# Performance work log

Hardware: AMD Instinct MI355X
Metric: run time of the kernel (lower is better)

Reference implementation:

```python
import jax, jax.numpy as jnp
import numpy as np

# Dimensions (TinyLlama-like)
B, T = 4, 1024
D = 2048          # hidden_size
H, DH = 32, 64    # heads, head_dim
HK = 8            # kv heads (GQA, n_rep = 4)
RQ, RKV = 32, 32  # per-head SVD ranks
RO, RF = 1024, 1024
I = 5632          # intermediate_size
THETA = 10000.0
EPS = 1e-5


def setup_inputs() -> dict:
    key = jax.random.key(0)
    ks = jax.random.split(key, 16)
    p = lambda k, s: jax.random.normal(k, s, jnp.float32) * 0.02
    return {
        "x": jax.random.normal(ks[0], (B, T, D), jnp.float32),
        "ln1_w": jnp.ones((D,), jnp.float32),
        "ln2_w": jnp.ones((D,), jnp.float32),
        "q_Us": p(ks[1], (H, DH, RQ)),  "q_V": p(ks[2], (H, RQ, D)),
        "k_Us": p(ks[3], (HK, DH, RKV)), "k_V": p(ks[4], (HK, RKV, D)),
        "v_Us": p(ks[5], (HK, DH, RKV)), "v_V": p(ks[6], (HK, RKV, D)),
        "o_Us": p(ks[7], (D, RO)),  "o_V": p(ks[8], (RO, H * DH)),
        "g_Us": p(ks[9], (I, RF)),  "g_V": p(ks[10], (RF, D)),
        "u_Us": p(ks[11], (I, RF)), "u_V": p(ks[12], (RF, D)),
        "d_Us": p(ks[13], (D, RF)), "d_V": p(ks[14], (RF, I)),
    }


def _rms(x, w):
    return x * jax.lax.rsqrt(jnp.mean(x * x, axis=-1, keepdims=True) + EPS) * w


def _rope_cos_sin(t_len, dh, dtype):
    half = dh // 2
    inv_freq = 1.0 / (THETA ** (jnp.arange(half, dtype=jnp.float32) / half))
    ang = jnp.arange(t_len, dtype=jnp.float32)[:, None] * inv_freq[None, :]  # [T, half]
    return jnp.cos(ang).astype(dtype), jnp.sin(ang).astype(dtype)


def _apply_rope(x, cos, sin):
    # x: [B,h,T,Dh], LLaMA half-split rotation
    half = x.shape[-1] // 2
    x1, x2 = x[..., :half], x[..., half:]
    c = cos[None, None]  # [1,1,T,half]
    s = sin[None, None]
    return jnp.concatenate([x1 * c - x2 * s, x2 * c + x1 * s], axis=-1)


def reference(x, ln1_w, ln2_w, q_Us, q_V, k_Us, k_V, v_Us, v_V,
              o_Us, o_V, g_Us, g_V, u_Us, u_V, d_Us, d_V):
    b, t, d = x.shape
    h1 = _rms(x, ln1_w)

    # per-head low-rank projections: y_h = x @ V_h^T @ Us_h^T
    q = jnp.einsum('bhtr,hdr->bhtd', jnp.einsum('btD,hrD->bhtr', h1, q_V), q_Us)  # [B,H,T,Dh]
    k = jnp.einsum('bhtr,hdr->bhtd', jnp.einsum('btD,hrD->bhtr', h1, k_V), k_Us)  # [B,Hk,T,Dh]
    v = jnp.einsum('bhtr,hdr->bhtd', jnp.einsum('btD,hrD->bhtr', h1, v_V), v_Us)

    cos, sin = _rope_cos_sin(t, DH, x.dtype)
    q = _apply_rope(q, cos, sin)
    k = _apply_rope(k, cos, sin)

    n_rep = H // HK
    k = jnp.repeat(k, n_rep, axis=1)  # _repeat_kv
    v = jnp.repeat(v, n_rep, axis=1)

    scale = 1.0 / np.sqrt(DH)
    scores = jnp.einsum('bhtd,bhsd->bhts', q, k) * scale
    causal = jnp.tril(jnp.ones((t, t), bool))
    scores = jnp.where(causal[None, None], scores, jnp.finfo(scores.dtype).min)
    attn = jax.nn.softmax(scores, axis=-1)
    ctx = jnp.einsum('bhts,bhsd->bhtd', attn, v)
    ctx = ctx.transpose(0, 2, 1, 3).reshape(b, t, H * DH)

    # low-rank output proj: o = ctx @ o_V^T @ o_Us^T
    attn_out = jnp.einsum('btr,Dr->btD', jnp.einsum('btk,rk->btr', ctx, o_V), o_Us)
    x = x + attn_out

    # SwiGLU MLP with low-rank factors
    h2 = _rms(x, ln2_w)
    g = jnp.einsum('btr,ir->bti', jnp.einsum('btD,rD->btr', h2, g_V), g_Us)
    u = jnp.einsum('btr,ir->bti', jnp.einsum('btD,rD->btr', h2, u_V), u_Us)
    ff = jax.nn.silu(g) * u
    down = jnp.einsum('btr,Dr->btD', jnp.einsum('bti,ri->btr', ff, d_V), d_Us)
    return x + down
```

## Files before the change

kernel.cpp:

```cpp
#include <hip/hip_runtime.h>
#include <math.h>

typedef unsigned short u16;
typedef unsigned int u32;
typedef __bf16 bf16x8 __attribute__((ext_vector_type(8)));
typedef float f32x4 __attribute__((ext_vector_type(4)));

__device__ __forceinline__ float bf2f(u16 u) {
  union { u32 i; float f; } x; x.i = ((u32)u) << 16; return x.f;
}
__device__ __forceinline__ u16 f2bf(float f) {
  union { float f; u32 i; } x; x.f = f;
  return (u16)((x.i + 0x7fffu + ((x.i >> 16) & 1u)) >> 16);
}

#define GLDS16(gp, lp)                                                        \
  __builtin_amdgcn_global_load_lds(                                           \
      (const __attribute__((address_space(1))) u32*)(gp),                     \
      (__attribute__((address_space(3))) u32*)(lp), 16, 0, 0)

__global__ void detect_k(const u16* __restrict__ w, int* __restrict__ flag) {
  if (threadIdx.x == 0 && blockIdx.x == 0)
    *flag = (w[0] == 0x0000u && w[1] == 0x3F80u) ? 1 : 0;
}

struct CvtArgs {
  const void* src[17];
  u32 dstOff[17];
  u32 blkOff[18];
};

__global__ __launch_bounds__(256) void cvt_all(CvtArgs a, u16* __restrict__ dstB,
                                               const int* __restrict__ flag) {
  int seg = 0;
  const int bx = blockIdx.x;
#pragma unroll 1
  while (bx >= (int)a.blkOff[seg + 1]) seg++;
  const long local = ((long)(bx - a.blkOff[seg]) * 256 + threadIdx.x) * 8;
  u16* dst = dstB + a.dstOff[seg] + local;
  if (*flag) {
    const float* s = (const float*)a.src[seg] + local;
    float4 va = *(const float4*)(s);
    float4 vb = *(const float4*)(s + 4);
    uint4 o; u16* op = (u16*)&o;
    op[0] = f2bf(va.x); op[1] = f2bf(va.y); op[2] = f2bf(va.z); op[3] = f2bf(va.w);
    op[4] = f2bf(vb.x); op[5] = f2bf(vb.y); op[6] = f2bf(vb.z); op[7] = f2bf(vb.w);
    *(uint4*)dst = o;
  } else {
    *(uint4*)dst = *(const uint4*)((const u16*)a.src[seg] + local);
  }
}

__global__ __launch_bounds__(256) void rms_k(const u16* __restrict__ x,
                                             const u16* __restrict__ w,
                                             u16* __restrict__ out) {
  const long row = blockIdx.x;
  const u16* xr = x + row * 2048;
  u16* orow = out + row * 2048;
  const int tid = threadIdx.x;
  const int base = tid * 8;
  uint4 u = *(const uint4*)(xr + base);
  const u16* us = (const u16*)&u;
  float v[8];
  float ss = 0.f;
#pragma unroll
  for (int i = 0; i < 8; i++) { v[i] = bf2f(us[i]); ss += v[i] * v[i]; }
#pragma unroll
  for (int off = 32; off > 0; off >>= 1) ss += __shfl_xor(ss, off);
  __shared__ float red[4];
  if ((tid & 63) == 0) red[tid >> 6] = ss;
  __syncthreads();
  float total = red[0] + red[1] + red[2] + red[3];
  float inv = rsqrtf(total * (1.0f / 2048.0f) + 1e-5f);
  uint4 wv = *(const uint4*)(w + base);
  const u16* wp = (const u16*)&wv;
  uint4 o;
  u16* op = (u16*)&o;
#pragma unroll
  for (int i = 0; i < 8; i++) op[i] = f2bf(v[i] * inv * bf2f(wp[i]));
  *(uint4*)(orow + base) = o;
}

template <int EPI>
__global__ __launch_bounds__(256, 2) void gemm_bt(const u16* __restrict__ A,
                                                  const u16* __restrict__ B,
                                                  void* Cv,
                                                  const u16* R,
                                                  const int* flagp,
                                                  int N, int Klen, int lda, int ldb) {
  __shared__ u16 As[128 * 32];
  __shared__ u16 Bs[128 * 32];
  const int m0 = blockIdx.y * 128;
  const int n0 = blockIdx.x * 128;
  const int tid = threadIdx.x;
  const int wave = tid >> 6;
  const int lane = tid & 63;
  const int wr = (wave >> 1) * 64;
  const int wc = (wave & 1) * 64;
  const int l16 = lane & 15;
  const int quad = lane >> 4;
  u16* C = (u16*)Cv;
  float* Cf = (float*)Cv;
  bool f32o = false;
  if (EPI == 3) f32o = (*flagp != 0);

  f32x4 acc[4][4];
#pragma unroll
  for (int i = 0; i < 4; i++)
#pragma unroll
    for (int j = 0; j < 4; j++) acc[i][j] = (f32x4){0.f, 0.f, 0.f, 0.f};

  const int srow = wave * 16 + (lane >> 2);
  const int scol = (lane & 3) * 8;
  const u16* Ag = A + (long)(m0 + srow) * lda + scol;
  const u16* Bg = B + (long)(n0 + srow) * ldb + scol;
  const long astep = (long)64 * lda;
  const long bstep = (long)64 * ldb;
  u16* Asw = &As[wave * 16 * 32];
  u16* Bsw = &Bs[wave * 16 * 32];

  for (int k0 = 0; k0 < Klen; k0 += 32) {
    GLDS16(Ag + k0, Asw);
    GLDS16(Ag + astep + k0, Asw + 64 * 32);
    GLDS16(Bg + k0, Bsw);
    GLDS16(Bg + bstep + k0, Bsw + 64 * 32);
    __syncthreads();
    bf16x8 af[4], bfr[4];
#pragma unroll
    for (int t = 0; t < 4; t++) {
      af[t]  = *(const bf16x8*)(&As[(wr + t * 16 + l16) * 32 + quad * 8]);
      bfr[t] = *(const bf16x8*)(&Bs[(wc + t * 16 + l16) * 32 + quad * 8]);
    }
#pragma unroll
    for (int i = 0; i < 4; i++)
#pragma unroll
      for (int j = 0; j < 4; j++)
        acc[i][j] = __builtin_amdgcn_mfma_f32_16x16x32_bf16(bfr[j], af[i], acc[i][j], 0, 0, 0);
    __syncthreads();
  }

#pragma unroll
  for (int i = 0; i < 4; i++) {
    const int m = m0 + wr + i * 16 + l16;
#pragma unroll
    for (int j = 0; j < 4; j++) {
      const int n = n0 + wc + j * 16 + quad * 4;
      const long idx = (long)m * N + n;
      float v[4];
#pragma unroll
      for (int r = 0; r < 4; r++) v[r] = acc[i][j][r];
      if (EPI == 1 || EPI == 3) {
        uint2 rr = *(const uint2*)(R + idx);
        const u16* rp = (const u16*)&rr;
#pragma unroll
        for (int r = 0; r < 4; r++) v[r] += bf2f(rp[r]);
      }
      if (EPI == 3 && f32o) {
        float4 o = {v[0], v[1], v[2], v[3]};
        *(float4*)(Cf + idx) = o;
      } else {
        uint2 o; u16* op = (u16*)&o;
#pragma unroll
        for (int r = 0; r < 4; r++) op[r] = f2bf(v[r]);
        *(uint2*)(C + idx) = o;
      }
    }
  }
}

#define STAGE_SILU(buf, k0)                                                   \
  do {                                                                        \
    GLDS16(Ag_ + (k0), &SH[buf][0][woff]);                                    \
    GLDS16(Au_ + (k0), &SH[buf][1][woff]);                                    \
    GLDS16(Bg_ + (k0), &SH[buf][2][woff]);                                    \
    GLDS16(Bu_ + (k0), &SH[buf][3][woff]);                                    \
  } while (0)

__global__ __launch_bounds__(512, 4) void gemm_silu(const u16* __restrict__ Agp,
                                                    const u16* __restrict__ Aup,
                                                    const u16* __restrict__ Bgp,
                                                    const u16* __restrict__ Bup,
                                                    u16* __restrict__ C,
                                                    int N, int Klen, int lda, int ldb) {
  __shared__ u16 SH[2][4][128 * 32];
  const int m0 = blockIdx.y * 128;
  const int n0 = blockIdx.x * 128;
  const int tid = threadIdx.x;
  const int wave = tid >> 6;
  const int lane = tid & 63;
  const int wid = wave & 3;
  const int isU = wave >> 2;
  const int wr = (wid >> 1) * 64;
  const int wc = (wid & 1) * 64;
  const int l16 = lane & 15;
  const int quad = lane >> 4;
  const int matA = isU;
  const int matB = 2 + isU;

  f32x4 acc[4][4];
#pragma unroll
  for (int i = 0; i < 4; i++)
#pragma unroll
    for (int j = 0; j < 4; j++) acc[i][j] = (f32x4){0.f, 0.f, 0.f, 0.f};

  const int srow = wave * 16 + (lane >> 2);
  const int scol = ((lane & 3) ^ ((lane >> 3) & 3)) * 8;
  const u16* Ag_ = Agp + (long)(m0 + srow) * lda + scol;
  const u16* Au_ = Aup + (long)(m0 + srow) * lda + scol;
  const u16* Bg_ = Bgp + (long)(n0 + srow) * ldb + scol;
  const u16* Bu_ = Bup + (long)(n0 + srow) * ldb + scol;
  const int woff = wave * 512;
  const int rsw = (quad ^ ((l16 >> 1) & 3)) * 8;

  const int nk = Klen >> 5;
  STAGE_SILU(0, 0);
  int cur = 0;
  for (int kt = 0; kt < nk; ++kt) {
    if (kt + 1 < nk) {
      STAGE_SILU(cur ^ 1, (kt + 1) << 5);
      asm volatile("s_waitcnt vmcnt(4)" ::: "memory");
    } else {
      asm volatile("s_waitcnt vmcnt(0)" ::: "memory");
    }
    asm volatile("s_barrier" ::: "memory");
    bf16x8 af[4], bfr[4];
#pragma unroll
    for (int t = 0; t < 4; t++) {
      af[t]  = *(const bf16x8*)(&SH[cur][matA][(wr + t * 16 + l16) * 32 + rsw]);
      bfr[t] = *(const bf16x8*)(&SH[cur][matB][(wc + t * 16 + l16) * 32 + rsw]);
    }
#pragma unroll
    for (int i = 0; i < 4; i++)
#pragma unroll
      for (int j = 0; j < 4; j++)
        acc[i][j] = __builtin_amdgcn_mfma_f32_16x16x32_bf16(bfr[j], af[i], acc[i][j], 0, 0, 0);
    asm volatile("s_barrier" ::: "memory");
    cur ^= 1;
  }

  float* xch = (float*)&SH[0][0][0];
  if (isU) {
    float* w = xch + wid * 4096 + lane * 4;
#pragma unroll
    for (int i = 0; i < 4; i++)
#pragma unroll
      for (int j = 0; j < 4; j++)
        *(f32x4*)(w + (i * 4 + j) * 256) = acc[i][j];
  }
  __syncthreads();
  if (!isU) {
    const float* w = xch + wid * 4096 + lane * 4;
#pragma unroll
    for (int i = 0; i < 4; i++) {
      const int m = m0 + wr + i * 16 + l16;
#pragma unroll
      for (int j = 0; j < 4; j++) {
        const int n = n0 + wc + j * 16 + quad * 4;
        const long idx = (long)m * N + n;
        f32x4 uv = *(const f32x4*)(w + (i * 4 + j) * 256);
        uint2 o; u16* op = (u16*)&o;
#pragma unroll
        for (int r = 0; r < 4; r++) {
          float g = acc[i][j][r];
          float v = uv[r] * g / (1.f + __expf(-g));
          op[r] = f2bf(v);
        }
        *(uint2*)(C + idx) = o;
      }
    }
  }
}

__global__ __launch_bounds__(256) void combine2(const u16* __restrict__ a,
                                                const u16* __restrict__ b,
                                                u16* __restrict__ o) {
  const long i = ((long)blockIdx.x * 256 + threadIdx.x) * 8;
  uint4 ua = *(const uint4*)(a + i);
  uint4 ub = *(const uint4*)(b + i);
  const u16* pa = (const u16*)&ua;
  const u16* pb = (const u16*)&ub;
  uint4 uo; u16* po = (u16*)&uo;
#pragma unroll
  for (int j = 0; j < 8; j++) po[j] = f2bf(bf2f(pa[j]) + bf2f(pb[j]));
  *(uint4*)(o + i) = uo;
}

__global__ __launch_bounds__(256) void expand_k(const u16* __restrict__ rbuf,
                                                int rstride,
                                                const u16* __restrict__ Us,
                                                u16* __restrict__ out,
                                                int nheads, int doRope) {
  const int tok = blockIdx.x;
  const int wave = threadIdx.x >> 6;
  const int d = threadIdx.x & 63;
  const int h = blockIdx.y * 4 + wave;
  const int b = tok >> 10;
  const int t = tok & 1023;
  const u16* up = Us + ((long)h * 64 + d) * 32;
  const u16* rp = rbuf + (long)tok * rstride + h * 32;
  float s = 0.f;
#pragma unroll
  for (int c = 0; c < 4; c++) {
    uint4 uu = *(const uint4*)(up + c * 8);
    uint4 rr = *(const uint4*)(rp + c * 8);
    const u16* u8p = (const u16*)&uu;
    const u16* r8p = (const u16*)&rr;
#pragma unroll
    for (int i = 0; i < 8; i++) s += bf2f(u8p[i]) * bf2f(r8p[i]);
  }
  if (doRope) {
    const int j = d & 31;
    float inv = powf(10000.0f, -(float)j * (1.0f / 32.0f));
    float ang = (float)t * inv;
    float sn, cs;
    sincosf(ang, &sn, &cs);
    float partner = __shfl_xor(s, 32);
    s = (d < 32) ? (s * cs - partner * sn) : (s * cs + partner * sn);
  }
  out[(((long)(b * nheads + h)) * 1024 + t) * 64 + d] = f2bf(s);
}

__global__ __launch_bounds__(256) void vT_k(const u16* __restrict__ vbuf,
                                            u16* __restrict__ vT) {
  __shared__ u16 tile[64][72];
  const int b = blockIdx.z, kh = blockIdx.y;
  const int t0 = blockIdx.x * 64;
  const int tid = threadIdx.x;
  const int r = tid >> 2;
  const int c = (tid & 3) * 16;
  const u16* src = vbuf + ((long)(b * 8 + kh) * 1024 + t0 + r) * 64 + c;
  *(uint4*)&tile[r][c] = *(const uint4*)src;
  *(uint4*)&tile[r][c + 8] = *(const uint4*)(src + 8);
  __syncthreads();
  u16 tmp[16];
#pragma unroll
  for (int i = 0; i < 16; i++) tmp[i] = tile[c + i][r];
  u16* dst = vT + ((long)(b * 8 + kh) * 64 + r) * 1024 + t0 + c;
  *(uint4*)dst = *(uint4*)&tmp[0];
  *(uint4*)(dst + 8) = *(uint4*)&tmp[8];
}

#define ATS 72

__global__ __launch_bounds__(256, 2) void attn_mfma(const u16* __restrict__ q,
                                                    const u16* __restrict__ k,
                                                    const u16* __restrict__ vT,
                                                    u16* __restrict__ ctx) {
  __shared__ u16 Ks[64 * ATS];
  __shared__ u16 Vts[64 * ATS];
  __shared__ u16 Plds[4][16 * ATS];
  const int bx = blockIdx.x;
  const int h = blockIdx.y;
  const int b = blockIdx.z;
  const int kh = h >> 2;
  const int qlo = bx * 64;
  const int qhi = (15 - bx) * 64;
  const int tid = threadIdx.x;
  const int wave = tid >> 6;
  const int lane = tid & 63;
  const int l16 = lane & 15;
  const int quad = lane >> 4;

  const u16* qb = q + ((long)(b * 32 + h) * 1024) * 64;
  const u16* kb = k + ((long)(b * 8 + kh) * 1024) * 64;
  const u16* vb = vT + ((long)(b * 8 + kh) * 64) * 1024;

  bf16x8 qfl[2], qfh[2];
  {
    const u16* qp = qb + (long)(qlo + wave * 16 + l16) * 64 + quad * 8;
    qfl[0] = *(const bf16x8*)(qp);
    qfl[1] = *(const bf16x8*)(qp + 32);
    qp = qb + (long)(qhi + wave * 16 + l16) * 64 + quad * 8;
    qfh[0] = *(const bf16x8*)(qp);
    qfh[1] = *(const bf16x8*)(qp + 32);
  }

  float ml[4], ll[4], mh[4], lh[4];
  f32x4 ol[4], oh[4];
#pragma unroll
  for (int r = 0; r < 4; r++) { ml[r] = -1e30f; ll[r] = 0.f; mh[r] = -1e30f; lh[r] = 0.f; }
#pragma unroll
  for (int j = 0; j < 4; j++) { ol[j] = (f32x4){0.f, 0.f, 0.f, 0.f}; oh[j] = ol[j]; }

  const int srow = tid >> 2;
  const int sc0 = (tid & 3) * 16;
  int s0 = 0;

  auto process = [&](const bf16x8* qf, float* m, float* l, f32x4* oacc, int qtb) {
    f32x4 s[4];
#pragma unroll
    for (int t = 0; t < 4; t++) {
      s[t] = (f32x4){0.f, 0.f, 0.f, 0.f};
      const u16* kr = &Ks[(t * 16 + l16) * ATS + quad * 8];
      bf16x8 b0 = *(const bf16x8*)(kr);
      bf16x8 b1 = *(const bf16x8*)(kr + 32);
      s[t] = __builtin_amdgcn_mfma_f32_16x16x32_bf16(qf[0], b0, s[t], 0, 0, 0);
      s[t] = __builtin_amdgcn_mfma_f32_16x16x32_bf16(qf[1], b1, s[t], 0, 0, 0);
    }
#pragma unroll
    for (int t = 0; t < 4; t++) s[t] *= 0.125f;
    if (s0 == qtb) {
#pragma unroll
      for (int t = 0; t < 4; t++)
#pragma unroll
        for (int r = 0; r < 4; r++)
          if (s0 + t * 16 + l16 > qtb + wave * 16 + quad * 4 + r) s[t][r] = -1e30f;
    }
    float p[4][4];
#pragma unroll
    for (int r = 0; r < 4; r++) {
      float mx = fmaxf(fmaxf(s[0][r], s[1][r]), fmaxf(s[2][r], s[3][r]));
#pragma unroll
      for (int off = 1; off < 16; off <<= 1) mx = fmaxf(mx, __shfl_xor(mx, off));
      const float mnew = fmaxf(m[r], mx);
      const float alpha = __expf(m[r] - mnew);
      float ps = 0.f;
#pragma unroll
      for (int t = 0; t < 4; t++) { p[t][r] = __expf(s[t][r] - mnew); ps += p[t][r]; }
#pragma unroll
      for (int off = 1; off < 16; off <<= 1) ps += __shfl_xor(ps, off);
      l[r] = l[r] * alpha + ps;
      m[r] = mnew;
#pragma unroll
      for (int j = 0; j < 4; j++) oacc[j][r] *= alpha;
    }
    u16* pw = &Plds[wave][0];
#pragma unroll
    for (int t = 0; t < 4; t++)
#pragma unroll
      for (int r = 0; r < 4; r++)
        pw[(quad * 4 + r) * ATS + t * 16 + l16] = f2bf(p[t][r]);
    bf16x8 pf0 = *(const bf16x8*)(&pw[l16 * ATS + quad * 8]);
    bf16x8 pf1 = *(const bf16x8*)(&pw[l16 * ATS + 32 + quad * 8]);
#pragma unroll
    for (int j = 0; j < 4; j++) {
      const u16* vr = &Vts[(j * 16 + l16) * ATS + quad * 8];
      bf16x8 v0 = *(const bf16x8*)(vr);
      bf16x8 v1 = *(const bf16x8*)(vr + 32);
      oacc[j] = __builtin_amdgcn_mfma_f32_16x16x32_bf16(pf0, v0, oacc[j], 0, 0, 0);
      oacc[j] = __builtin_amdgcn_mfma_f32_16x16x32_bf16(pf1, v1, oacc[j], 0, 0, 0);
    }
  };

  for (s0 = 0; s0 <= qhi; s0 += 64) {
    __syncthreads();
    {
      const u16* kp = kb + (long)(s0 + srow) * 64 + sc0;
      *(uint4*)&Ks[srow * ATS + sc0] = *(const uint4*)kp;
      *(uint4*)&Ks[srow * ATS + sc0 + 8] = *(const uint4*)(kp + 8);
      const u16* vp = vb + (long)srow * 1024 + s0 + sc0;
      *(uint4*)&Vts[srow * ATS + sc0] = *(const uint4*)vp;
      *(uint4*)&Vts[srow * ATS + sc0 + 8] = *(const uint4*)(vp + 8);
    }
    __syncthreads();
    process(qfh, mh, lh, oh, qhi);
    if (s0 <= qlo) process(qfl, ml, ll, ol, qlo);
  }

#pragma unroll
  for (int r = 0; r < 4; r++) {
    const int rowl = qlo + wave * 16 + quad * 4 + r;
    const int rowh = qhi + wave * 16 + quad * 4 + r;
    const float il = 1.f / ll[r];
    const float ih = 1.f / lh[r];
#pragma unroll
    for (int j = 0; j < 4; j++) {
      ctx[(((long)(b * 1024 + rowl)) * 32 + h) * 64 + j * 16 + l16] = f2bf(ol[j][r] * il);
      ctx[(((long)(b * 1024 + rowh)) * 32 + h) * 64 + j * 16 + l16] = f2bf(oh[j][r] * ih);
    }
  }
}

extern "C" void kernel_launch(void* const* d_in, const int* in_sizes, int n_in,
                              void* d_out, int out_size, void* d_ws, size_t ws_size,
                              hipStream_t stream) {
  char* ws = (char*)d_ws;
  u16* cb = (u16*)ws;
  u16* cx    = cb + 0;
  u16* cln1  = cb + 8388608;
  u16* cln2  = cb + 8390656;
  u16* cqUs  = cb + 8392704;
  u16* ckUs  = cb + 8458240;
  u16* cvUs  = cb + 8474624;
  u16* cqkvV = cb + 8491008;
  u16* coUs  = cb + 11636736;
  u16* coV   = cb + 13733888;
  u16* cguV  = cb + 15831040;
  u16* cgUs  = cb + 20025344;
  u16* cuUs  = cb + 25792512;
  u16* cdUs  = cb + 31559680;
  u16* cdV   = cb + 33656832;

  char* P = ws + 78848000;
  u16* h1    = (u16*)(P + 0);
  u16* qkvr  = (u16*)(P + 16777216);
  u16* qp0   = (u16*)(P + 33554432);
  u16* qp1   = (u16*)(P + 46137344);
  u16* qbuf  = (u16*)(P + 33554432);
  u16* kbuf  = (u16*)(P + 50331648);
  u16* vbuf  = (u16*)(P + 54525952);
  u16* ctx   = (u16*)(P + 58720256);
  u16* vbufT = (u16*)(P + 75497472);
  u16* orr   = (u16*)(P + 75497472);
  u16* xmid  = (u16*)(P + 83886080);
  u16* op0   = (u16*)(P + 0);
  u16* op1   = (u16*)(P + 8388608);
  u16* h2    = (u16*)(P + 0);
  u16* gur   = (u16*)(P + 16777216);
  u16* gbuf  = (u16*)(P + 33554432);
  u16* dp0   = (u16*)(P + 0);
  u16* dp1   = (u16*)(P + 8388608);
  u16* dr    = (u16*)(P + 16777216);
  int* flag  = (int*)(ws + 179511296);

  const dim3 blk(256);
  detect_k<<<1, 64, 0, stream>>>((const u16*)d_in[1], flag);

  CvtArgs ca;
  const u32 dOff[17] = {0u, 8388608u, 8390656u, 8392704u, 8491008u, 8458240u,
                        10588160u, 8474624u, 11112448u, 11636736u, 13733888u,
                        20025344u, 15831040u, 25792512u, 17928192u, 31559680u,
                        33656832u};
  const u32 nblk[17] = {4096u, 1u, 1u, 32u, 1024u, 8u, 256u, 8u, 256u, 1024u,
                        1024u, 2816u, 1024u, 2816u, 1024u, 1024u, 2816u};
  u32 cum = 0;
  for (int i = 0; i < 17; i++) {
    ca.src[i] = d_in[i];
    ca.dstOff[i] = dOff[i];
    ca.blkOff[i] = cum;
    cum += nblk[i];
  }
  ca.blkOff[17] = cum;
  cvt_all<<<cum, blk, 0, stream>>>(ca, cb, flag);

  rms_k<<<4096, blk, 0, stream>>>(cx, cln1, h1);
  gemm_bt<0><<<dim3(12, 32), blk, 0, stream>>>(h1, cqkvV, qp0, nullptr, nullptr, 1536, 1024, 2048, 2048);
  gemm_bt<0><<<dim3(12, 32), blk, 0, stream>>>(h1 + 1024, cqkvV + 1024, qp1, nullptr, nullptr, 1536, 1024, 2048, 2048);
  combine2<<<3072, blk, 0, stream>>>(qp0, qp1, qkvr);
  expand_k<<<dim3(4096, 8), blk, 0, stream>>>(qkvr, 1536, cqUs, qbuf, 32, 1);
  expand_k<<<dim3(4096, 2), blk, 0, stream>>>(qkvr + 1024, 1536, ckUs, kbuf, 8, 1);
  expand_k<<<dim3(4096, 2), blk, 0, stream>>>(qkvr + 1280, 1536, cvUs, vbuf, 8, 0);
  vT_k<<<dim3(16, 8, 4), blk, 0, stream>>>(vbuf, vbufT);
  attn_mfma<<<dim3(8, 32, 4), blk, 0, stream>>>(qbuf, kbuf, vbufT, ctx);
  gemm_bt<0><<<dim3(8, 32), blk, 0, stream>>>(ctx, coV, op0, nullptr, nullptr, 1024, 1024, 2048, 2048);
  gemm_bt<0><<<dim3(8, 32), blk, 0, stream>>>(ctx + 1024, coV + 1024, op1, nullptr, nullptr, 1024, 1024, 2048, 2048);
  combine2<<<2048, blk, 0, stream>>>(op0, op1, orr);
  gemm_bt<1><<<dim3(16, 32), blk, 0, stream>>>(orr, coUs, xmid, cx, nullptr, 2048, 1024, 1024, 1024);
  rms_k<<<4096, blk, 0, stream>>>(xmid, cln2, h2);
  gemm_bt<0><<<dim3(16, 32), blk, 0, stream>>>(h2, cguV, gur, nullptr, nullptr, 2048, 2048, 2048, 2048);
  gemm_silu<<<dim3(44, 32), dim3(512), 0, stream>>>(gur, gur + 1024, cgUs, cuUs, gbuf, 5632, 1024, 2048, 1024);
  gemm_bt<0><<<dim3(8, 32), blk, 0, stream>>>(gbuf, cdV, dp0, nullptr, nullptr, 1024, 2816, 5632, 5632);
  gemm_bt<0><<<dim3(8, 32), blk, 0, stream>>>(gbuf + 2816, cdV + 2816, dp1, nullptr, nullptr, 1024, 2816, 5632, 5632);
  combine2<<<2048, blk, 0, stream>>>(dp0, dp1, dr);
  gemm_bt<3><<<dim3(16, 32), blk, 0, stream>>>(dr, cdUs, d_out, xmid, flag, 2048, 1024, 1024, 1024);
}
```

Before: 851.8 us.

## Replace fused gate/up SiLU GEMM with two 256x256-tile pipelined GEMMs

The fused 128x128 gemm_silu kernel is replaced by a new 256x256-tile, 8-wave GEMM with 128KB of dynamic LDS, a BK=64 double buffer, loads staggered between MFMA phases and s_setprio. The up projection is computed first into gbuf. A second launch computes the gate projection and applies SiLU(g)*u, reading the stored up values from gbuf in place. The aim is more data reuse per tile and better overlap of loads with MFMAs, paid for by an extra bf16 round-trip of the up output through global memory and fewer blocks (352 per launch).

Measured after the change: 889.0 us. +4.4%, slower.

```diff
diff --git a/kernel.cpp b/kernel.cpp
--- a/kernel.cpp
+++ b/kernel.cpp
@@ -168,107 +168,170 @@
   }
 }
 
-#define STAGE_SILU(buf, k0)                                                   \
-  do {                                                                        \
-    GLDS16(Ag_ + (k0), &SH[buf][0][woff]);                                    \
-    GLDS16(Au_ + (k0), &SH[buf][1][woff]);                                    \
-    GLDS16(Bg_ + (k0), &SH[buf][2][woff]);                                    \
-    GLDS16(Bu_ + (k0), &SH[buf][3][woff]);                                    \
-  } while (0)
-
-__global__ __launch_bounds__(512, 4) void gemm_silu(const u16* __restrict__ Agp,
-                                                    const u16* __restrict__ Aup,
-                                                    const u16* __restrict__ Bgp,
-                                                    const u16* __restrict__ Bup,
-                                                    u16* __restrict__ C,
-                                                    int N, int Klen, int lda, int ldb) {
-  __shared__ u16 SH[2][4][128 * 32];
-  const int m0 = blockIdx.y * 128;
-  const int n0 = blockIdx.x * 128;
+template <int EPI>
+__global__ __launch_bounds__(512, 2) void gemm256(const u16* __restrict__ A,
+                                                  const u16* __restrict__ B,
+                                                  u16* C,
+                                                  const u16* partner,
+                                                  int N, int Klen, int lda, int ldb) {
+  extern __shared__ u16 lds[];
+  u16* Abase = lds;
+  u16* Bbase = lds + 32768;
+  const int m0 = blockIdx.y * 256;
+  const int n0 = blockIdx.x * 256;
   const int tid = threadIdx.x;
   const int wave = tid >> 6;
   const int lane = tid & 63;
-  const int wid = wave & 3;
-  const int isU = wave >> 2;
-  const int wr = (wid >> 1) * 64;
-  const int wc = (wid & 1) * 64;
+  const int wm = wave >> 2;
+  const int wn = wave & 3;
   const int l16 = lane & 15;
   const int quad = lane >> 4;
-  const int matA = isU;
-  const int matB = 2 + isU;
-
-  f32x4 acc[4][4];
-#pragma unroll
-  for (int i = 0; i < 4; i++)
+
+  f32x4 acc[8][4];
+#pragma unroll
+  for (int i = 0; i < 8; i++)
 #pragma unroll
     for (int j = 0; j < 4; j++) acc[i][j] = (f32x4){0.f, 0.f, 0.f, 0.f};
 
-  const int srow = wave * 16 + (lane >> 2);
-  const int scol = ((lane & 3) ^ ((lane >> 3) & 3)) * 8;
-  const u16* Ag_ = Agp + (long)(m0 + srow) * lda + scol;
-  const u16* Au_ = Aup + (long)(m0 + srow) * lda + scol;
-  const u16* Bg_ = Bgp + (long)(n0 + srow) * ldb + scol;
-  const u16* Bu_ = Bup + (long)(n0 + srow) * ldb + scol;
-  const int woff = wave * 512;
-  const int rsw = (quad ^ ((l16 >> 1) & 3)) * 8;
-
-  const int nk = Klen >> 5;
-  STAGE_SILU(0, 0);
-  int cur = 0;
-  for (int kt = 0; kt < nk; ++kt) {
-    if (kt + 1 < nk) {
-      STAGE_SILU(cur ^ 1, (kt + 1) << 5);
-      asm volatile("s_waitcnt vmcnt(4)" ::: "memory");
-    } else {
-      asm volatile("s_waitcnt vmcnt(0)" ::: "memory");
-    }
-    asm volatile("s_barrier" ::: "memory");
-    bf16x8 af[4], bfr[4];
-#pragma unroll
-    for (int t = 0; t < 4; t++) {
-      af[t]  = *(const bf16x8*)(&SH[cur][matA][(wr + t * 16 + l16) * 32 + rsw]);
-      bfr[t] = *(const bf16x8*)(&SH[cur][matB][(wc + t * 16 + l16) * 32 + rsw]);
-    }
+  const int srow = tid >> 3;
+  const int sg = (tid & 7) ^ ((tid >> 4) & 7);
+  const u16* Asrc = A + (long)(m0 + srow) * lda + sg * 8;
+  const u16* Bsrc = B + (long)(n0 + srow) * ldb + sg * 8;
+
+#define STH(MATBASE, SRC, LD, buf, h, k0)                                     \
+  do {                                                                        \
+    GLDS16(SRC + (long)((h) * 128) * (LD) + (k0),                             \
+           MATBASE + ((buf) * 2 + (h)) * 8192 + wave * 512);                  \
+    GLDS16(SRC + (long)((h) * 128 + 64) * (LD) + (k0),                        \
+           MATBASE + ((buf) * 2 + (h)) * 8192 + 4096 + wave * 512);           \
+  } while (0)
+
+#define RDA(buf, r, g16) \
+  (*(const bf16x8*)(Abase + (((buf) * 2 + wm) * 128 + (r)) * 64 + (((g16) ^ (((r) >> 1) & 7)) * 8)))
+#define RDB(buf, r, g16) \
+  (*(const bf16x8*)(Bbase + (((buf) * 2 + (wn >> 1)) * 128 + (r)) * 64 + (((g16) ^ (((r) >> 1) & 7)) * 8)))
+
+  const int nt = Klen >> 6;
+  const int rb = (wn & 1) * 64;
+
+  STH(Abase, Asrc, lda, 0, 0, 0);
+  STH(Abase, Asrc, lda, 0, 1, 0);
+  STH(Bbase, Bsrc, ldb, 0, 0, 0);
+  STH(Bbase, Bsrc, ldb, 0, 1, 0);
+  STH(Abase, Asrc, lda, 1, 0, 64);
+
+  for (int t = 0; t < nt; ++t) {
+    const int buf = t & 1;
+    const int nbuf = buf ^ 1;
+    const int k1 = (t + 1) << 6;
+    const int k2 = (t + 2) << 6;
+    if (t < nt - 1) asm volatile("s_waitcnt vmcnt(2)" ::: "memory");
+    else            asm volatile("s_waitcnt vmcnt(0)" ::: "memory");
+    __builtin_amdgcn_s_barrier();
+    bf16x8 a0[4][2], b0[2][2];
+#pragma unroll
+    for (int i = 0; i < 4; i++) {
+      a0[i][0] = RDA(buf, i * 16 + l16, quad);
+      a0[i][1] = RDA(buf, i * 16 + l16, 4 + quad);
+    }
+#pragma unroll
+    for (int j = 0; j < 2; j++) {
+      b0[j][0] = RDB(buf, rb + j * 16 + l16, quad);
+      b0[j][1] = RDB(buf, rb + j * 16 + l16, 4 + quad);
+    }
+    if (t + 1 < nt) STH(Abase, Asrc, lda, nbuf, 1, k1);
+    __builtin_amdgcn_s_barrier();
+    asm volatile("s_waitcnt lgkmcnt(0)" ::: "memory");
+    __builtin_amdgcn_sched_barrier(0);
+    __builtin_amdgcn_s_setprio(1);
 #pragma unroll
     for (int i = 0; i < 4; i++)
 #pragma unroll
-      for (int j = 0; j < 4; j++)
-        acc[i][j] = __builtin_amdgcn_mfma_f32_16x16x32_bf16(bfr[j], af[i], acc[i][j], 0, 0, 0);
-    asm volatile("s_barrier" ::: "memory");
-    cur ^= 1;
-  }
-
-  float* xch = (float*)&SH[0][0][0];
-  if (isU) {
-    float* w = xch + wid * 4096 + lane * 4;
+      for (int j = 0; j < 2; j++) {
+        acc[i][j] = __builtin_amdgcn_mfma_f32_16x16x32_bf16(b0[j][0], a0[i][0], acc[i][j], 0, 0, 0);
+        acc[i][j] = __builtin_amdgcn_mfma_f32_16x16x32_bf16(b0[j][1], a0[i][1], acc[i][j], 0, 0, 0);
+      }
+    __builtin_amdgcn_s_setprio(0);
+    __builtin_amdgcn_s_barrier();
+    bf16x8 b1[2][2];
+#pragma unroll
+    for (int j = 0; j < 2; j++) {
+      b1[j][0] = RDB(buf, rb + (j + 2) * 16 + l16, quad);
+      b1[j][1] = RDB(buf, rb + (j + 2) * 16 + l16, 4 + quad);
+    }
+    if (t + 1 < nt) STH(Bbase, Bsrc, ldb, nbuf, 0, k1);
+    __builtin_amdgcn_s_barrier();
+    asm volatile("s_waitcnt lgkmcnt(0)" ::: "memory");
+    __builtin_amdgcn_sched_barrier(0);
+    __builtin_amdgcn_s_setprio(1);
 #pragma unroll
     for (int i = 0; i < 4; i++)
 #pragma unroll
-      for (int j = 0; j < 4; j++)
-        *(f32x4*)(w + (i * 4 + j) * 256) = acc[i][j];
-  }
-  __syncthreads();
-  if (!isU) {
-    const float* w = xch + wid * 4096 + lane * 4;
+      for (int j = 0; j < 2; j++) {
+        acc[i][j + 2] = __builtin_amdgcn_mfma_f32_16x16x32_bf16(b1[j][0], a0[i][0], acc[i][j + 2], 0, 0, 0);
+        acc[i][j + 2] = __builtin_amdgcn_mfma_f32_16x16x32_bf16(b1[j][1], a0[i][1], acc[i][j + 2], 0, 0, 0);
+      }
+    __builtin_amdgcn_s_setprio(0);
+    __builtin_amdgcn_s_barrier();
+    bf16x8 a1[4][2];
 #pragma unroll
     for (int i = 0; i < 4; i++) {
-      const int m = m0 + wr + i * 16 + l16;
-#pragma unroll
-      for (int j = 0; j < 4; j++) {
-        const int n = n0 + wc + j * 16 + quad * 4;
-        const long idx = (long)m * N + n;
-        f32x4 uv = *(const f32x4*)(w + (i * 4 + j) * 256);
-        uint2 o; u16* op = (u16*)&o;
+      a1[i][0] = RDA(buf, (i + 4) * 16 + l16, quad);
+      a1[i][1] = RDA(buf, (i + 4) * 16 + l16, 4 + quad);
+    }
+    if (t + 1 < nt) STH(Bbase, Bsrc, ldb, nbuf, 1, k1);
+    __builtin_amdgcn_s_barrier();
+    asm volatile("s_waitcnt lgkmcnt(0)" ::: "memory");
+    __builtin_amdgcn_sched_barrier(0);
+    __builtin_amdgcn_s_setprio(1);
+#pragma unroll
+    for (int i = 0; i < 4; i++)
+#pragma unroll
+      for (int j = 0; j < 2; j++) {
+        acc[i + 4][j] = __builtin_amdgcn_mfma_f32_16x16x32_bf16(b0[j][0], a1[i][0], acc[i + 4][j], 0, 0, 0);
+        acc[i + 4][j] = __builtin_amdgcn_mfma_f32_16x16x32_bf16(b0[j][1], a1[i][1], acc[i + 4][j], 0, 0, 0);
+      }
+    __builtin_amdgcn_s_setprio(0);
+    __builtin_amdgcn_s_barrier();
+    if (t + 2 < nt) STH(Abase, Asrc, lda, buf, 0, k2);
+    __builtin_amdgcn_s_setprio(1);
+#pragma unroll
+    for (int i = 0; i < 4; i++)
+#pragma unroll
+      for (int j = 0; j < 2; j++) {
+        acc[i + 4][j + 2] = __builtin_amdgcn_mfma_f32_16x16x32_bf16(b1[j][0], a1[i][0], acc[i + 4][j + 2], 0, 0, 0);
+        acc[i + 4][j + 2] = __builtin_amdgcn_mfma_f32_16x16x32_bf16(b1[j][1], a1[i][1], acc[i + 4][j + 2], 0, 0, 0);
+      }
+    __builtin_amdgcn_s_setprio(0);
+  }
+
+#pragma unroll
+  for (int i = 0; i < 8; i++) {
+    const int m = m0 + wm * 128 + i * 16 + l16;
+#pragma unroll
+    for (int j = 0; j < 4; j++) {
+      const int n = n0 + wn * 64 + j * 16 + quad * 4;
+      const long idx = (long)m * N + n;
+      uint2 o; u16* op = (u16*)&o;
+      if (EPI == 4) {
+        uint2 up = *(const uint2*)(partner + idx);
+        const u16* upp = (const u16*)&up;
 #pragma unroll
         for (int r = 0; r < 4; r++) {
           float g = acc[i][j][r];
-          float v = uv[r] * g / (1.f + __expf(-g));
+          float v = bf2f(upp[r]) * g / (1.f + __expf(-g));
           op[r] = f2bf(v);
         }
-        *(uint2*)(C + idx) = o;
+      } else {
+#pragma unroll
+        for (int r = 0; r < 4; r++) op[r] = f2bf(acc[i][j][r]);
       }
-    }
-  }
+      *(uint2*)(C + idx) = o;
+    }
+  }
+#undef STH
+#undef RDA
+#undef RDB
 }
 
 __global__ __launch_bounds__(256) void combine2(const u16* __restrict__ a,
@@ -513,6 +576,15 @@
   u16* dr    = (u16*)(P + 16777216);
   int* flag  = (int*)(ws + 179511296);
 
+  static bool attrDone = false;
+  if (!attrDone) {
+    hipFuncSetAttribute(reinterpret_cast<const void*>(&gemm256<0>),
+                        hipFuncAttributeMaxDynamicSharedMemorySize, 131072);
+    hipFuncSetAttribute(reinterpret_cast<const void*>(&gemm256<4>),
+                        hipFuncAttributeMaxDynamicSharedMemorySize, 131072);
+    attrDone = true;
+  }
+
   const dim3 blk(256);
   detect_k<<<1, 64, 0, stream>>>((const u16*)d_in[1], flag);
 
@@ -548,7 +620,8 @@
   gemm_bt<1><<<dim3(16, 32), blk, 0, stream>>>(orr, coUs, xmid, cx, nullptr, 2048, 1024, 1024, 1024);
   rms_k<<<4096, blk, 0, stream>>>(xmid, cln2, h2);
   gemm_bt<0><<<dim3(16, 32), blk, 0, stream>>>(h2, cguV, gur, nullptr, nullptr, 2048, 2048, 2048, 2048);
-  gemm_silu<<<dim3(44, 32), dim3(512), 0, stream>>>(gur, gur + 1024, cgUs, cuUs, gbuf, 5632, 1024, 2048, 1024);
+  gemm256<0><<<dim3(22, 16), dim3(512), 131072, stream>>>(gur + 1024, cuUs, gbuf, nullptr, 5632, 1024, 2048, 1024);
+  gemm256<4><<<dim3(22, 16), dim3(512), 131072, stream>>>(gur, cgUs, gbuf, gbuf, 5632, 1024, 2048, 1024);
   gemm_bt<0><<<dim3(8, 32), blk, 0, stream>>>(gbuf, cdV, dp0, nullptr, nullptr, 1024, 2816, 5632, 5632);
   gemm_bt<0><<<dim3(8, 32), blk, 0, stream>>>(gbuf + 2816, cdV + 2816, dp1, nullptr, nullptr, 1024, 2816, 5632, 5632);
   combine2<<<2048, blk, 0, stream>>>(dp0, dp1, dr);
```

## Fuse first RMSNorm into convert, merge split-K GEMMs, precompute RoPE table

Applied to the files above, without the earlier changes.

Folds the first RMSNorm into the input-conversion kernel for the x segment, so h1 is written without a separate pass. The paired split-K GEMM launches become single launches that use blockIdx.z to pick the K half and output buffer. RoPE cos/sin values now come from a precomputed table instead of powf/sincosf per element. The GEMM launch bound changes from 2 to 3 blocks per SM, which may limit registers and cause spills.

After: 768.1 us. 1.11x faster.

```diff
diff --git a/kernel.cpp b/kernel.cpp
--- a/kernel.cpp
+++ b/kernel.cpp
@@ -22,6 +22,16 @@
 __global__ void detect_k(const u16* __restrict__ w, int* __restrict__ flag) {
   if (threadIdx.x == 0 && blockIdx.x == 0)
     *flag = (w[0] == 0x0000u && w[1] == 0x3F80u) ? 1 : 0;
+}
+
+__global__ __launch_bounds__(256) void rope_tab_k(float2* __restrict__ tab) {
+  const int idx = blockIdx.x * 256 + threadIdx.x;
+  const int t = idx >> 5, j = idx & 31;
+  float inv = powf(10000.0f, -(float)j * (1.0f / 32.0f));
+  float ang = (float)t * inv;
+  float sn, cs;
+  sincosf(ang, &sn, &cs);
+  tab[idx] = make_float2(cs, sn);
 }
 
 struct CvtArgs {
@@ -31,23 +41,60 @@
 };
 
 __global__ __launch_bounds__(256) void cvt_all(CvtArgs a, u16* __restrict__ dstB,
-                                               const int* __restrict__ flag) {
+                                               const int* __restrict__ flag,
+                                               const void* __restrict__ w1src,
+                                               u16* __restrict__ h1) {
   int seg = 0;
   const int bx = blockIdx.x;
 #pragma unroll 1
   while (bx >= (int)a.blkOff[seg + 1]) seg++;
-  const long local = ((long)(bx - a.blkOff[seg]) * 256 + threadIdx.x) * 8;
+  const int tid = threadIdx.x;
+  const long local = ((long)(bx - a.blkOff[seg]) * 256 + tid) * 8;
   u16* dst = dstB + a.dstOff[seg] + local;
-  if (*flag) {
+  const bool f32in = (*flag != 0);
+  uint4 o; u16* op = (u16*)&o;
+  if (f32in) {
     const float* s = (const float*)a.src[seg] + local;
     float4 va = *(const float4*)(s);
     float4 vb = *(const float4*)(s + 4);
-    uint4 o; u16* op = (u16*)&o;
     op[0] = f2bf(va.x); op[1] = f2bf(va.y); op[2] = f2bf(va.z); op[3] = f2bf(va.w);
     op[4] = f2bf(vb.x); op[5] = f2bf(vb.y); op[6] = f2bf(vb.z); op[7] = f2bf(vb.w);
-    *(uint4*)dst = o;
   } else {
-    *(uint4*)dst = *(const uint4*)((const u16*)a.src[seg] + local);
+    o = *(const uint4*)((const u16*)a.src[seg] + local);
+  }
+  *(uint4*)dst = o;
+
+  if (seg == 0) {
+    float v[8];
+    float ss = 0.f;
+#pragma unroll
+    for (int i = 0; i < 8; i++) { v[i] = bf2f(op[i]); ss += v[i] * v[i]; }
+#pragma unroll
+    for (int off = 32; off > 0; off >>= 1) ss += __shfl_xor(ss, off);
+    __shared__ float red[4];
+    if ((tid & 63) == 0) red[tid >> 6] = ss;
+    __syncthreads();
+    const float total = red[0] + red[1] + red[2] + red[3];
+    const float inv = rsqrtf(total * (1.0f / 2048.0f) + 1e-5f);
+    float wv[8];
+    if (f32in) {
+      const float* wp = (const float*)w1src + tid * 8;
+      float4 wa = *(const float4*)(wp);
+      float4 wb = *(const float4*)(wp + 4);
+      wv[0] = bf2f(f2bf(wa.x)); wv[1] = bf2f(f2bf(wa.y));
+      wv[2] = bf2f(f2bf(wa.z)); wv[3] = bf2f(f2bf(wa.w));
+      wv[4] = bf2f(f2bf(wb.x)); wv[5] = bf2f(f2bf(wb.y));
+      wv[6] = bf2f(f2bf(wb.z)); wv[7] = bf2f(f2bf(wb.w));
+    } else {
+      uint4 ww = *((const uint4*)w1src + tid);
+      const u16* wp = (const u16*)&ww;
+#pragma unroll
+      for (int i = 0; i < 8; i++) wv[i] = bf2f(wp[i]);
+    }
+    uint4 ho; u16* hop = (u16*)&ho;
+#pragma unroll
+    for (int i = 0; i < 8; i++) hop[i] = f2bf(v[i] * inv * wv[i]);
+    *(uint4*)(h1 + (long)bx * 2048 + tid * 8) = ho;
   }
 }
 
@@ -82,14 +129,19 @@
 }
 
 template <int EPI>
-__global__ __launch_bounds__(256, 2) void gemm_bt(const u16* __restrict__ A,
+__global__ __launch_bounds__(256, 3) void gemm_bt(const u16* __restrict__ A,
                                                   const u16* __restrict__ B,
                                                   void* Cv,
+                                                  void* Cv2,
                                                   const u16* R,
                                                   const int* flagp,
                                                   int N, int Klen, int lda, int ldb) {
   __shared__ u16 As[128 * 32];
   __shared__ u16 Bs[128 * 32];
+  const long koff = (long)blockIdx.z * Klen;
+  A += koff;
+  B += koff;
+  if (blockIdx.z) Cv = Cv2;
   const int m0 = blockIdx.y * 128;
   const int n0 = blockIdx.x * 128;
   const int tid = threadIdx.x;
@@ -289,6 +341,7 @@
                                                 int rstride,
                                                 const u16* __restrict__ Us,
                                                 u16* __restrict__ out,
+                                                const float2* __restrict__ tab,
                                                 int nheads, int doRope) {
   const int tok = blockIdx.x;
   const int wave = threadIdx.x >> 6;
@@ -310,12 +363,9 @@
   }
   if (doRope) {
     const int j = d & 31;
-    float inv = powf(10000.0f, -(float)j * (1.0f / 32.0f));
-    float ang = (float)t * inv;
-    float sn, cs;
-    sincosf(ang, &sn, &cs);
+    float2 cs2 = tab[(t << 5) | j];
     float partner = __shfl_xor(s, 32);
-    s = (d < 32) ? (s * cs - partner * sn) : (s * cs + partner * sn);
+    s = (d < 32) ? (s * cs2.x - partner * cs2.y) : (s * cs2.x + partner * cs2.y);
   }
   out[(((long)(b * nheads + h)) * 1024 + t) * 64 + d] = f2bf(s);
 }
@@ -511,10 +561,12 @@
   u16* dp0   = (u16*)(P + 0);
   u16* dp1   = (u16*)(P + 8388608);
   u16* dr    = (u16*)(P + 16777216);
+  float2* ropetab = (float2*)(P + 79691776);
   int* flag  = (int*)(ws + 179511296);
 
   const dim3 blk(256);
   detect_k<<<1, 64, 0, stream>>>((const u16*)d_in[1], flag);
+  rope_tab_k<<<128, blk, 0, stream>>>(ropetab);
 
   CvtArgs ca;
   const u32 dOff[17] = {0u, 8388608u, 8390656u, 8392704u, 8491008u, 8458240u,
@@ -531,26 +583,22 @@
     cum += nblk[i];
   }
   ca.blkOff[17] = cum;
-  cvt_all<<<cum, blk, 0, stream>>>(ca, cb, flag);
-
-  rms_k<<<4096, blk, 0, stream>>>(cx, cln1, h1);
-  gemm_bt<0><<<dim3(12, 32), blk, 0, stream>>>(h1, cqkvV, qp0, nullptr, nullptr, 1536, 1024, 2048, 2048);
-  gemm_bt<0><<<dim3(12, 32), blk, 0, stream>>>(h1 + 1024, cqkvV + 1024, qp1, nullptr, nullptr, 1536, 1024, 2048, 2048);
+  cvt_all<<<cum, blk, 0, stream>>>(ca, cb, flag, d_in[1], h1);
+
+  gemm_bt<0><<<dim3(12, 32, 2), blk, 0, stream>>>(h1, cqkvV, qp0, qp1, nullptr, nullptr, 1536, 1024, 2048, 2048);
   combine2<<<3072, blk, 0, stream>>>(qp0, qp1, qkvr);
-  expand_k<<<dim3(4096, 8), blk, 0, stream>>>(qkvr, 1536, cqUs, qbuf, 32, 1);
-  expand_k<<<dim3(4096, 2), blk, 0, stream>>>(qkvr + 1024, 1536, ckUs, kbuf, 8, 1);
-  expand_k<<<dim3(4096, 2), blk, 0, stream>>>(qkvr + 1280, 1536, cvUs, vbuf, 8, 0);
+  expand_k<<<dim3(4096, 8), blk, 0, stream>>>(qkvr, 1536, cqUs, qbuf, ropetab, 32, 1);
+  expand_k<<<dim3(4096, 2), blk, 0, stream>>>(qkvr + 1024, 1536, ckUs, kbuf, ropetab, 8, 1);
+  expand_k<<<dim3(4096, 2), blk, 0, stream>>>(qkvr + 1280, 1536, cvUs, vbuf, ropetab, 8, 0);
   vT_k<<<dim3(16, 8, 4), blk, 0, stream>>>(vbuf, vbufT);
   attn_mfma<<<dim3(8, 32, 4), blk, 0, stream>>>(qbuf, kbuf, vbufT, ctx);
-  gemm_bt<0><<<dim3(8, 32), blk, 0, stream>>>(ctx, coV, op0, nullptr, nullptr, 1024, 1024, 2048, 2048);
-  gemm_bt<0><<<dim3(8, 32), blk, 0, stream>>>(ctx + 1024, coV + 1024, op1, nullptr, nullptr, 1024, 1024, 2048, 2048);
+  gemm_bt<0><<<dim3(8, 32, 2), blk, 0, stream>>>(ctx, coV, op0, op1, nullptr, nullptr, 1024, 1024, 2048, 2048);
   combine2<<<2048, blk, 0, stream>>>(op0, op1, orr);
-  gemm_bt<1><<<dim3(16, 32), blk, 0, stream>>>(orr, coUs, xmid, cx, nullptr, 2048, 1024, 1024, 1024);
+  gemm_bt<1><<<dim3(16, 32), blk, 0, stream>>>(orr, coUs, xmid, nullptr, cx, nullptr, 2048, 1024, 1024, 1024);
   rms_k<<<4096, blk, 0, stream>>>(xmid, cln2, h2);
-  gemm_bt<0><<<dim3(16, 32), blk, 0, stream>>>(h2, cguV, gur, nullptr, nullptr, 2048, 2048, 2048, 2048);
+  gemm_bt<0><<<dim3(16, 32), blk, 0, stream>>>(h2, cguV, gur, nullptr, nullptr, nullptr, 2048, 2048, 2048, 2048);
   gemm_silu<<<dim3(44, 32), dim3(512), 0, stream>>>(gur, gur + 1024, cgUs, cuUs, gbuf, 5632, 1024, 2048, 1024);
-  gemm_bt<0><<<dim3(8, 32), blk, 0, stream>>>(gbuf, cdV, dp0, nullptr, nullptr, 1024, 2816, 5632, 5632);
-  gemm_bt<0><<<dim3(8, 32), blk, 0, stream>>>(gbuf + 2816, cdV + 2816, dp1, nullptr, nullptr, 1024, 2816, 5632, 5632);
+  gemm_bt<0><<<dim3(8, 32, 2), blk, 0, stream>>>(gbuf, cdV, dp0, dp1, nullptr, nullptr, 1024, 2816, 5632, 5632);
   combine2<<<2048, blk, 0, stream>>>(dp0, dp1, dr);
-  gemm_bt<3><<<dim3(16, 32), blk, 0, stream>>>(dr, cdUs, d_out, xmid, flag, 2048, 1024, 1024, 1024);
-}
+  gemm_bt<3><<<dim3(16, 32), blk, 0, stream>>>(dr, cdUs, d_out, nullptr, xmid, flag, 2048, 1024, 1024, 1024);
+}
```
